# Optimization experiments

Hardware: AMD Instinct MI355X
Metric: run time of the kernel (lower is better)

The kernel has to match this reference:

```python
import jax, jax.numpy as jnp
import numpy as np
from jax import lax

B, ROWS, COLS, K, LATENT = 8, 1536, 16, 32, 16
EPS_REG = 0.01  # torchsort regularization_strength
BIG = 1e30


def setup_inputs() -> dict:
    key = jax.random.key(0)
    ks = jax.random.split(key, 12)
    def w(k, shape):
        return (jax.random.normal(k, shape, jnp.float32) / np.sqrt(shape[0])).astype(jnp.float32)
    return {
        "table": jax.random.uniform(ks[0], (B, ROWS, COLS), jnp.float32),
        "enc_w1": w(ks[1], (COLS, 32)), "enc_b1": 0.01 * jax.random.normal(ks[2], (32,), jnp.float32),
        "enc_w2": w(ks[3], (32, 64)),   "enc_b2": 0.01 * jax.random.normal(ks[4], (64,), jnp.float32),
        "mean_w": w(ks[5], (64, LATENT)), "mean_b": 0.01 * jax.random.normal(ks[6], (LATENT,), jnp.float32),
        "dec_w1": w(ks[7], (LATENT, 32)), "dec_b1": 0.01 * jax.random.normal(ks[8], (32,), jnp.float32),
        "dec_w2": w(ks[9], (32, COLS)),   "dec_b2": 0.01 * jax.random.normal(ks[10], (COLS,), jnp.float32),
        "labels": jax.random.randint(ks[11], (ROWS,), 0, K, jnp.int32),
        "BlockSize": 64,
        "current_epoch": 0,
        "baseline": 0,
    }


def _soft_rank_l2(s, eps):
    # Exact soft_rank (Blondel et al. / torchsort, l2 reg, ascending):
    # project s/eps onto permutahedron of (n,...,1).
    n = s.shape[0]
    x = s / eps
    perm = jnp.argsort(-x)            # descending sort
    xs = x[perm]
    w = jnp.arange(n, 0, -1, dtype=x.dtype)
    # dual = non-increasing isotonic fit of y = xs - w == -iso_inc(-(xs - w))
    y = -(xs - w)
    S = jnp.concatenate([jnp.zeros((1,), x.dtype), jnp.cumsum(y)])
    idx = jnp.arange(n)
    length = jnp.maximum(idx[None, :] - idx[:, None] + 1, 1).astype(x.dtype)
    A = (S[1:][None, :] - S[:n][:, None]) / length           # mean(y[j..k])  [j,k]
    A = jnp.where(idx[None, :] >= idx[:, None], A, BIG)
    Bm = lax.cummin(A, axis=1, reverse=True)                  # min_{k>=i} A[j,k]
    Cm = lax.cummax(Bm, axis=0)                               # max_{j<=i} ...
    iso_inc = jnp.diagonal(Cm)
    dual = -iso_inc
    primal = xs - dual
    inv = jnp.argsort(perm)
    return primal[inv]


def _forward(table, enc_w1, enc_b1, enc_w2, enc_b2, mean_w, mean_b,
             dec_w1, dec_b1, dec_w2, dec_b2, labels, BlockSize):
    b = table.shape[0]
    # VAE (autoencoder path; z = latent mean)
    h = jax.nn.relu(table @ enc_w1 + enc_b1)
    h = jax.nn.relu(h @ enc_w2 + enc_b2)
    z = h @ mean_w + mean_b                                   # [B, rows, 16]
    r = jax.nn.relu(z @ dec_w1 + dec_b1)
    recon = jax.nn.relu(r @ dec_w2 + dec_b2)
    loss = jnp.mean((recon - table) ** 2)
    # clustering scores (labels fixed from batch 0, shared across batch)
    onehot = jax.nn.one_hot(labels, K, dtype=z.dtype)         # [rows, K]
    counts = jnp.maximum(onehot.sum(0), 1.0)                  # [K]
    centers = jnp.einsum('brd,rk->bkd', z, onehot) / counts[None, :, None]
    center_data = centers[:, labels, :]                       # gather back [B, rows, 16]
    d2 = jnp.mean((z - center_data) ** 2, axis=-1)            # [B, rows]
    mn = d2.min(axis=1, keepdims=True); mx = d2.max(axis=1, keepdims=True)
    d2 = (d2 - mn) / (mx - mn)
    scores = d2 + labels.astype(z.dtype)[None, :]
    # training branch
    smn = scores.min(axis=1, keepdims=True); smx = scores.max(axis=1, keepdims=True)
    scaled = (scores - smn) / (smx - smn) * jnp.asarray(b, z.dtype)  # * len(table)
    ranks = jax.vmap(lambda s: _soft_rank_l2(s, EPS_REG))(scaled)
    rank_idx = jnp.argsort(jnp.argsort(scores, axis=1), axis=1) // BlockSize + 1
    rows = table.shape[1]
    return (ranks.reshape(b, rows, 1), rank_idx.reshape(b, rows, 1),
            scores.reshape(b, rows, 1), loss)


def reference(table, enc_w1, enc_b1, enc_w2, enc_b2, mean_w, mean_b,
              dec_w1, dec_b1, dec_w2, dec_b2, labels, BlockSize,
              current_epoch, baseline):
    return _forward(table, enc_w1, enc_b1, enc_w2, enc_b2, mean_w, mean_b,
                    dec_w1, dec_b1, dec_w2, dec_b2, labels, BlockSize)
```

## Files before the change

### kernel.cpp

```cpp
#include <hip/hip_runtime.h>

#define BATCH 8
#define ROWS 1536
#define KCLS 32
#define NTOT (BATCH*ROWS)
#define ELEMS (NTOT*16)
#define SSTRIDE 3073
#define BIGF 1.0e30f

enum : int {
  WS_Z     = 0,
  WS_X     = WS_Z + NTOT*16,
  WS_XS    = WS_X + NTOT,
  WS_S     = WS_XS + NTOT,
  WS_DESC  = WS_S + BATCH*SSTRIDE,
  WS_ASCP  = WS_DESC + NTOT,
  WS_DSCP  = WS_ASCP + 4*NTOT,
  WS_GPART = WS_DSCP + 4*NTOT,
  WS_LOSSP = WS_GPART + BATCH*8*ROWS,
};
#define WS_CPART WS_GPART

#define LW1  0
#define LB1  512
#define LW2  544
#define LB2  2592
#define LMW  2656
#define LMB  3680
#define LDW1 3696
#define LDB1 4208
#define LDW2 4240
#define LDB2 4752
#define LTOT 4768

#define AX   0
#define AH1  16
#define AH2  48
#define AZ   112
#define AR1  128
#define AREC 144
#define ATOT 160
#define ASTRIDE 164

template<int IN_BASE, int IN_N, int OUT_BASE, int OUT_PW, int OUT_TOT,
         int WOFF, int BOFF, bool RELU>
__device__ __forceinline__ void layerw(float* __restrict__ act,
                                       const float* __restrict__ wsh,
                                       int lrow, int wav)
{
  const int o0 = wav * OUT_PW;
  float acc[OUT_PW];
#pragma unroll
  for (int j = 0; j < OUT_PW; ++j) acc[j] = wsh[BOFF + o0 + j];

  const float4* arow = reinterpret_cast<const float4*>(&act[lrow*ASTRIDE + IN_BASE]);
#pragma unroll 2
  for (int i4 = 0; i4 < IN_N/4; ++i4) {
    float4 sv = arow[i4];
    float svx[4];
    svx[0] = sv.x; svx[1] = sv.y; svx[2] = sv.z; svx[3] = sv.w;
#pragma unroll
    for (int u = 0; u < 4; ++u) {
      const float s = svx[u];
      const float4* wp =
        reinterpret_cast<const float4*>(&wsh[WOFF + (i4*4 + u)*OUT_TOT + o0]);
#pragma unroll
      for (int q = 0; q < OUT_PW/4; ++q) {
        float4 w = wp[q];
        acc[q*4+0] = fmaf(s, w.x, acc[q*4+0]);
        acc[q*4+1] = fmaf(s, w.y, acc[q*4+1]);
        acc[q*4+2] = fmaf(s, w.z, acc[q*4+2]);
        acc[q*4+3] = fmaf(s, w.w, acc[q*4+3]);
      }
    }
  }
  float4* orow = reinterpret_cast<float4*>(&act[lrow*ASTRIDE + OUT_BASE + o0]);
#pragma unroll
  for (int q = 0; q < OUT_PW/4; ++q) {
    float4 v;
    v.x = RELU ? fmaxf(acc[q*4+0], 0.f) : acc[q*4+0];
    v.y = RELU ? fmaxf(acc[q*4+1], 0.f) : acc[q*4+1];
    v.z = RELU ? fmaxf(acc[q*4+2], 0.f) : acc[q*4+2];
    v.w = RELU ? fmaxf(acc[q*4+3], 0.f) : acc[q*4+3];
    orow[q] = v;
  }
}

__global__ __launch_bounds__(256, 2) void k1_ae(
    const float* __restrict__ table,
    const float* __restrict__ w1, const float* __restrict__ b1,
    const float* __restrict__ w2, const float* __restrict__ b2,
    const float* __restrict__ mw, const float* __restrict__ mb,
    const float* __restrict__ dw1, const float* __restrict__ db1,
    const float* __restrict__ dw2, const float* __restrict__ db2,
    const int* __restrict__ labels,
    float* __restrict__ ws)
{
  const int tid  = threadIdx.x;
  const int lrow = tid & 63;
  const int wav  = tid >> 6;
  const int blk  = blockIdx.x;
  const int b    = blk / 24;
  const int ch   = blk % 24;

  __shared__ float wsh[LTOT];
  __shared__ float act[64 * ASTRIDE];
  __shared__ int   lbl[64];
  __shared__ float lred[4];

  {
    float4* d4 = reinterpret_cast<float4*>(wsh);
#define CPY(off, src, nf4) \
    { const float4* p = reinterpret_cast<const float4*>(src); \
      for (int t = tid; t < (nf4); t += 256) d4[(off)/4 + t] = p[t]; }
    CPY(LW1,  w1,  128) CPY(LB1,  b1,  8)  CPY(LW2,  w2,  512)
    CPY(LB2,  b2,  16)  CPY(LMW,  mw,  256) CPY(LMB,  mb,  4)
    CPY(LDW1, dw1, 128) CPY(LDB1, db1, 8)  CPY(LDW2, dw2, 128)
    CPY(LDB2, db2, 4)
#undef CPY
    if (tid < 64) lbl[tid] = labels[ch * 64 + tid];
    const float4* tp = reinterpret_cast<const float4*>(table) + blk*256 + tid;
    float4* a4 = reinterpret_cast<float4*>(act);
    a4[(tid >> 2) * (ASTRIDE/4) + (tid & 3)] = *tp;
  }
  __syncthreads();

  layerw<AX,  16, AH1,  8, 32, LW1,  LB1,  true >(act, wsh, lrow, wav);
  __syncthreads();
  layerw<AH1, 32, AH2, 16, 64, LW2,  LB2,  true >(act, wsh, lrow, wav);
  __syncthreads();
  layerw<AH2, 64, AZ,   4, 16, LMW,  LMB,  false>(act, wsh, lrow, wav);
  __syncthreads();

  {
    const float4* a4 = reinterpret_cast<const float4*>(act);
    float4 zv = a4[(tid >> 2) * (ASTRIDE/4) + (AZ/4) + (tid & 3)];
    reinterpret_cast<float4*>(ws + WS_Z)[blk*256 + tid] = zv;
  }

  layerw<AZ,  16, AR1,  8, 32, LDW1, LDB1, true >(act, wsh, lrow, wav);
  __syncthreads();
  layerw<AR1, 32, AREC, 4, 16, LDW2, LDB2, true >(act, wsh, lrow, wav);
  __syncthreads();

  {
    const float4* arow4 = reinterpret_cast<const float4*>(&act[lrow*ASTRIDE]);
    float4 rc = arow4[AREC/4 + wav];
    float4 xv = arow4[AX/4 + wav];
    float d0 = rc.x - xv.x, d1 = rc.y - xv.y, d2 = rc.z - xv.z, d3 = rc.w - xv.w;
    float ls = d0*d0 + d1*d1 + d2*d2 + d3*d3;
    for (int off = 32; off > 0; off >>= 1) ls += __shfl_down(ls, off);
    if (lrow == 0) lred[wav] = ls;
    __syncthreads();
    if (tid == 0) ws[WS_LOSSP + blk] = (lred[0] + lred[1]) + (lred[2] + lred[3]);
  }

  {
    float a0 = 0.f, a1 = 0.f;
    const int d0 = tid & 15,        k0 = tid >> 4;
    const int k1c = k0 + 16;
    for (int rr = 0; rr < 64; ++rr) {
      const int lb = lbl[rr];
      const float zv = act[rr*ASTRIDE + AZ + d0];
      a0 += (lb == k0)  ? zv : 0.f;
      a1 += (lb == k1c) ? zv : 0.f;
    }
    ws[WS_CPART + (b*24 + ch)*512 + tid]       = a0;
    ws[WS_CPART + (b*24 + ch)*512 + 256 + tid] = a1;
  }
}

__global__ __launch_bounds__(256) void k345(const int* __restrict__ labels,
                                            float* __restrict__ ws,
                                            float* __restrict__ out)
{
  const int b = blockIdx.x;
  const int tid = threadIdx.x;
  __shared__ int cnt[KCLS];
  __shared__ float cent[512];
  __shared__ float rmn[256], rmx[256];
  __shared__ int lbl_l[ROWS];

  rmn[tid] = (tid < 192) ? ws[WS_LOSSP + tid] : 0.f;
  if (tid < KCLS) cnt[tid] = 0;
  __syncthreads();
  for (int off = 128; off > 0; off >>= 1) {
    if (tid < off) rmn[tid] += rmn[tid + off];
    __syncthreads();
  }
  if (b == 0 && tid == 0) out[3*NTOT] = rmn[0] / (float)ELEMS;

#pragma unroll
  for (int c = 0; c < 6; ++c) {
    int lb = labels[c*256 + tid];
    lbl_l[c*256 + tid] = lb;
    atomicAdd(&cnt[lb], 1);
  }
  __syncthreads();
#pragma unroll
  for (int e = tid; e < 512; e += 256) {
    float s = 0.f;
#pragma unroll
    for (int c = 0; c < 24; ++c) s += ws[WS_CPART + (b*24 + c)*512 + e];
    const int cn = cnt[e >> 4] > 1 ? cnt[e >> 4] : 1;
    cent[e] = s / (float)cn;
  }
  __syncthreads();

  float d2v[6];
  float tmn = 3.0e38f, tmx = -3.0e38f;
#pragma unroll
  for (int c = 0; c < 6; ++c) {
    const int r = c*256 + tid;
    const int lb = lbl_l[r];
    const float4* zp = reinterpret_cast<const float4*>(ws + WS_Z + (b*ROWS + r)*16);
    const float4* cp = reinterpret_cast<const float4*>(&cent[lb*16]);
    float s = 0.f;
#pragma unroll
    for (int q = 0; q < 4; ++q) {
      float4 zv = zp[q], cv = cp[q];
      float d0 = zv.x - cv.x, d1 = zv.y - cv.y, d2_ = zv.z - cv.z, d3 = zv.w - cv.w;
      s += d0*d0 + d1*d1 + d2_*d2_ + d3*d3;
    }
    d2v[c] = s / 16.f;
    tmn = fminf(tmn, d2v[c]); tmx = fmaxf(tmx, d2v[c]);
  }
  rmn[tid] = tmn; rmx[tid] = tmx;
  __syncthreads();
  for (int off = 128; off > 0; off >>= 1) {
    if (tid < off) {
      rmn[tid] = fminf(rmn[tid], rmn[tid + off]);
      rmx[tid] = fmaxf(rmx[tid], rmx[tid + off]);
    }
    __syncthreads();
  }
  const float mn = rmn[0], mx = rmx[0];
  __syncthreads();

  float sv[6];
  tmn = 3.0e38f; tmx = -3.0e38f;
#pragma unroll
  for (int c = 0; c < 6; ++c) {
    const int r = c*256 + tid;
    float sc = (d2v[c] - mn) / (mx - mn) + (float)lbl_l[r];
    sv[c] = sc;
    out[2*NTOT + b*ROWS + r] = sc;
    tmn = fminf(tmn, sc); tmx = fmaxf(tmx, sc);
  }
  rmn[tid] = tmn; rmx[tid] = tmx;
  __syncthreads();
  for (int off = 128; off > 0; off >>= 1) {
    if (tid < off) {
      rmn[tid] = fminf(rmn[tid], rmn[tid + off]);
      rmx[tid] = fmaxf(rmx[tid], rmx[tid + off]);
    }
    __syncthreads();
  }
  const float smn = rmn[0], smx = rmx[0];
#pragma unroll
  for (int c = 0; c < 6; ++c) {
    const int r = c*256 + tid;
    float scl = (sv[c] - smn) / (smx - smn) * 8.0f;
    ws[WS_X + b*ROWS + r] = scl / 0.01f;
  }
}

__global__ __launch_bounds__(256) void k6_count(float* __restrict__ ws,
                                                const float* __restrict__ out)
{
  const int bi = blockIdx.x;
  const int jb = bi & 3, rb = (bi >> 2) % 6, b = bi / 24;
  const int tid = threadIdx.x;
  __shared__ float4 sld[96], xld[96];
  {
    float* sf = reinterpret_cast<float*>(sld);
    float* xf = reinterpret_cast<float*>(xld);
    const int base = b*ROWS + jb*384;
    sf[tid] = out[2*NTOT + base + tid];
    xf[tid] = ws[WS_X + base + tid];
    if (tid < 128) {
      sf[256 + tid] = out[2*NTOT + base + 256 + tid];
      xf[256 + tid] = ws[WS_X + base + 256 + tid];
    }
  }
  __syncthreads();
  const int r = rb*256 + tid;
  const float si = out[2*NTOT + b*ROWS + r];
  const float xi = ws[WS_X + b*ROWS + r];
  int asc = 0, dsc = 0;
  const int j0 = jb*384;
#pragma unroll 4
  for (int kk = 0; kk < 96; ++kk) {
    const float4 s4 = sld[kk];
    const float4 x4 = xld[kk];
    const int j = j0 + kk*4;
    asc += (s4.x < si || (s4.x == si && j   < r)) ? 1 : 0;
    asc += (s4.y < si || (s4.y == si && j+1 < r)) ? 1 : 0;
    asc += (s4.z < si || (s4.z == si && j+2 < r)) ? 1 : 0;
    asc += (s4.w < si || (s4.w == si && j+3 < r)) ? 1 : 0;
    dsc += (x4.x > xi || (x4.x == xi && j   < r)) ? 1 : 0;
    dsc += (x4.y > xi || (x4.y == xi && j+1 < r)) ? 1 : 0;
    dsc += (x4.z > xi || (x4.z == xi && j+2 < r)) ? 1 : 0;
    dsc += (x4.w > xi || (x4.w == xi && j+3 < r)) ? 1 : 0;
  }
  int* wsi = reinterpret_cast<int*>(ws);
  wsi[WS_ASCP + jb*NTOT + b*ROWS + r] = asc;
  wsi[WS_DSCP + jb*NTOT + b*ROWS + r] = dsc;
}

__global__ __launch_bounds__(256) void k67(const int* __restrict__ bsp,
                                           float* __restrict__ ws,
                                           float* __restrict__ out)
{
  const int b = blockIdx.x, tid = threadIdx.x;
  __shared__ float xs_l[ROWS];
  __shared__ float ts[256];
  const int* wsi = reinterpret_cast<const int*>(ws);
  int* wsw = reinterpret_cast<int*>(ws);
  const int BS = *bsp;
#pragma unroll
  for (int c = 0; c < 6; ++c) {
    const int r = c*256 + tid;
    const int idx = b*ROWS + r;
    int asc = 0, dsc = 0;
#pragma unroll
    for (int jb = 0; jb < 4; ++jb) {
      asc += wsi[WS_ASCP + jb*NTOT + idx];
      dsc += wsi[WS_DSCP + jb*NTOT + idx];
    }
    out[NTOT + idx] = (float)(asc / BS + 1);
    wsw[WS_DESC + idx] = dsc;
    xs_l[dsc] = ws[WS_X + idx];
  }
  __syncthreads();
  const int base = tid * 6;
  float y[6], sum = 0.f;
#pragma unroll
  for (int u = 0; u < 6; ++u) {
    ws[WS_XS + b*ROWS + base + u] = xs_l[base + u];
    y[u] = (float)(ROWS - (base + u)) - xs_l[base + u];
    sum += y[u];
  }
  ts[tid] = sum;
  __syncthreads();
  for (int off = 1; off < 256; off <<= 1) {
    float v = ts[tid];
    if (tid >= off) v += ts[tid - off];
    __syncthreads();
    ts[tid] = v;
    __syncthreads();
  }
  float run = tid ? ts[tid - 1] : 0.f;
  float* S = ws + WS_S + b*SSTRIDE;
#pragma unroll
  for (int u = 0; u < 6; ++u) { S[base + u] = run; run += y[u]; }
  if (tid == 255) S[ROWS] = run;
#pragma unroll
  for (int u = 0; u < 6; ++u) S[ROWS + 1 + tid*6 + u] = BIGF;
}

__global__ __launch_bounds__(256) void k8a(float* __restrict__ ws)
{
  const int bi = blockIdx.x;
  const int c = bi & 7, ib = (bi >> 3) % 6, b = bi / 48;
  const int tid = threadIdx.x;
  __shared__ float Sseg[448];
  __shared__ float invl[192];
  const float* S = ws + WS_S + b*SSTRIDE;
  const int ibase = ib*256;
  const int segbase = ibase + c*192 + 1;
  Sseg[tid] = S[segbase + tid];
  if (tid < 192) {
    Sseg[256 + tid] = S[segbase + 256 + tid];
    invl[tid] = 1.0f / (float)(c*192 + tid + 1);
  }
  __syncthreads();
  const int i = ibase + tid;
  const float Si = S[i];
  float gm = 3.0e38f;
#pragma unroll 8
  for (int k = 0; k < 192; ++k)
    gm = fminf(gm, (Sseg[tid + k] - Si) * invl[k]);
  ws[WS_GPART + (b*8 + c)*ROWS + i] = gm;
}

__global__ __launch_bounds__(768) void k8b(float* __restrict__ ws,
                                           float* __restrict__ out)
{
  const int b = blockIdx.x, tid = threadIdx.x;
  __shared__ float g[ROWS];
  __shared__ float pm[768];
  for (int t = tid; t < ROWS; t += 768) {
    float gm = 3.0e38f;
#pragma unroll
    for (int c = 0; c < 8; ++c)
      gm = fminf(gm, ws[WS_GPART + (b*8 + c)*ROWS + t]);
    g[t] = gm;
  }
  __syncthreads();
  const float a = g[2*tid], cc = g[2*tid + 1];
  pm[tid] = fmaxf(a, cc);
  __syncthreads();
  for (int off = 1; off < 768; off <<= 1) {
    float v = pm[tid];
    if (tid >= off) v = fmaxf(v, pm[tid - off]);
    __syncthreads();
    pm[tid] = v;
    __syncthreads();
  }
  const float excl = tid ? pm[tid - 1] : -3.0e38f;
  const float i0 = fmaxf(excl, a);
  const float i1 = fmaxf(i0, cc);
  g[2*tid] = i0; g[2*tid + 1] = i1;
  __syncthreads();
  const float* xs = ws + WS_XS + b*ROWS;
  const int* desc = reinterpret_cast<const int*>(ws) + WS_DESC + b*ROWS;
  for (int t = tid; t < ROWS; t += 768) {
    const int dr = desc[t];
    out[b*ROWS + t] = xs[dr] + g[dr];
  }
}

extern "C" void kernel_launch(void* const* d_in, const int* in_sizes, int n_in,
                              void* d_out, int out_size, void* d_ws, size_t ws_size,
                              hipStream_t stream) {
  const float* table = (const float*)d_in[0];
  const float* w1  = (const float*)d_in[1];
  const float* b1  = (const float*)d_in[2];
  const float* w2  = (const float*)d_in[3];
  const float* b2  = (const float*)d_in[4];
  const float* mw  = (const float*)d_in[5];
  const float* mb  = (const float*)d_in[6];
  const float* dw1 = (const float*)d_in[7];
  const float* db1 = (const float*)d_in[8];
  const float* dw2 = (const float*)d_in[9];
  const float* db2 = (const float*)d_in[10];
  const int* labels = (const int*)d_in[11];
  const int* bsp    = (const int*)d_in[12];
  float* out = (float*)d_out;
  float* ws  = (float*)d_ws;

  k1_ae<<<192, 256, 0, stream>>>(table, w1, b1, w2, b2, mw, mb, dw1, db1, dw2, db2, labels, ws);
  k345<<<8, 256, 0, stream>>>(labels, ws, out);
  k6_count<<<192, 256, 0, stream>>>(ws, out);
  k67<<<8, 256, 0, stream>>>(bsp, ws, out);
  k8a<<<384, 256, 0, stream>>>(ws);
  k8b<<<8, 768, 0, stream>>>(ws, out);
}
```

Before: 62.71 us.

## Split autoencoder kernel into 16-row blocks to quadruple grid size

The autoencoder kernel now handles 16 rows per block with 16 threads per output slice, instead of 64 rows with 4 waves, so it launches 768 blocks rather than 192. The aim is to fill more of the GPU's compute units and shorten the per-block serial work in the small MLP layers. In exchange, every block reloads the full weight set into shared memory, and the downstream kernel has to sum 96 per-chunk centroid partials and 768 loss partials instead of 24 and 192. The workspace layout grows to hold the extra partial sums.

```diff
diff --git a/kernel.cpp b/kernel.cpp
--- a/kernel.cpp
+++ b/kernel.cpp
@@ -17,7 +17,7 @@
   WS_ASCP  = WS_DESC + NTOT,
   WS_DSCP  = WS_ASCP + 4*NTOT,
   WS_GPART = WS_DSCP + 4*NTOT,
-  WS_LOSSP = WS_GPART + BATCH*8*ROWS,
+  WS_LOSSP = WS_GPART + BATCH*96*512,
 };
 #define WS_CPART WS_GPART
 
@@ -42,13 +42,16 @@
 #define ATOT 160
 #define ASTRIDE 164
 
+#define RPB 16
+#define FWAYS 16
+
 template<int IN_BASE, int IN_N, int OUT_BASE, int OUT_PW, int OUT_TOT,
          int WOFF, int BOFF, bool RELU>
 __device__ __forceinline__ void layerw(float* __restrict__ act,
                                        const float* __restrict__ wsh,
-                                       int lrow, int wav)
-{
-  const int o0 = wav * OUT_PW;
+                                       int lrow, int fway)
+{
+  const int o0 = fway * OUT_PW;
   float acc[OUT_PW];
 #pragma unroll
   for (int j = 0; j < OUT_PW; ++j) acc[j] = wsh[BOFF + o0 + j];
@@ -62,31 +65,47 @@
 #pragma unroll
     for (int u = 0; u < 4; ++u) {
       const float s = svx[u];
-      const float4* wp =
-        reinterpret_cast<const float4*>(&wsh[WOFF + (i4*4 + u)*OUT_TOT + o0]);
-#pragma unroll
-      for (int q = 0; q < OUT_PW/4; ++q) {
-        float4 w = wp[q];
-        acc[q*4+0] = fmaf(s, w.x, acc[q*4+0]);
-        acc[q*4+1] = fmaf(s, w.y, acc[q*4+1]);
-        acc[q*4+2] = fmaf(s, w.z, acc[q*4+2]);
-        acc[q*4+3] = fmaf(s, w.w, acc[q*4+3]);
+      const float* wp = &wsh[WOFF + (i4*4 + u)*OUT_TOT + o0];
+      if constexpr (OUT_PW == 1) {
+        acc[0] = fmaf(s, wp[0], acc[0]);
+      } else if constexpr (OUT_PW == 2) {
+        float2 w = *reinterpret_cast<const float2*>(wp);
+        acc[0] = fmaf(s, w.x, acc[0]);
+        acc[1] = fmaf(s, w.y, acc[1]);
+      } else {
+#pragma unroll
+        for (int q = 0; q < OUT_PW/4; ++q) {
+          float4 w = reinterpret_cast<const float4*>(wp)[q];
+          acc[q*4+0] = fmaf(s, w.x, acc[q*4+0]);
+          acc[q*4+1] = fmaf(s, w.y, acc[q*4+1]);
+          acc[q*4+2] = fmaf(s, w.z, acc[q*4+2]);
+          acc[q*4+3] = fmaf(s, w.w, acc[q*4+3]);
+        }
       }
     }
   }
-  float4* orow = reinterpret_cast<float4*>(&act[lrow*ASTRIDE + OUT_BASE + o0]);
-#pragma unroll
-  for (int q = 0; q < OUT_PW/4; ++q) {
-    float4 v;
-    v.x = RELU ? fmaxf(acc[q*4+0], 0.f) : acc[q*4+0];
-    v.y = RELU ? fmaxf(acc[q*4+1], 0.f) : acc[q*4+1];
-    v.z = RELU ? fmaxf(acc[q*4+2], 0.f) : acc[q*4+2];
-    v.w = RELU ? fmaxf(acc[q*4+3], 0.f) : acc[q*4+3];
-    orow[q] = v;
-  }
-}
-
-__global__ __launch_bounds__(256, 2) void k1_ae(
+  float* orow = &act[lrow*ASTRIDE + OUT_BASE + o0];
+  if constexpr (OUT_PW == 1) {
+    orow[0] = RELU ? fmaxf(acc[0], 0.f) : acc[0];
+  } else if constexpr (OUT_PW == 2) {
+    float2 v;
+    v.x = RELU ? fmaxf(acc[0], 0.f) : acc[0];
+    v.y = RELU ? fmaxf(acc[1], 0.f) : acc[1];
+    *reinterpret_cast<float2*>(orow) = v;
+  } else {
+#pragma unroll
+    for (int q = 0; q < OUT_PW/4; ++q) {
+      float4 v;
+      v.x = RELU ? fmaxf(acc[q*4+0], 0.f) : acc[q*4+0];
+      v.y = RELU ? fmaxf(acc[q*4+1], 0.f) : acc[q*4+1];
+      v.z = RELU ? fmaxf(acc[q*4+2], 0.f) : acc[q*4+2];
+      v.w = RELU ? fmaxf(acc[q*4+3], 0.f) : acc[q*4+3];
+      reinterpret_cast<float4*>(orow)[q] = v;
+    }
+  }
+}
+
+__global__ __launch_bounds__(256, 4) void k1_ae(
     const float* __restrict__ table,
     const float* __restrict__ w1, const float* __restrict__ b1,
     const float* __restrict__ w2, const float* __restrict__ b2,
@@ -97,15 +116,15 @@
     float* __restrict__ ws)
 {
   const int tid  = threadIdx.x;
-  const int lrow = tid & 63;
-  const int wav  = tid >> 6;
+  const int lrow = tid & (RPB-1);
+  const int fway = tid >> 4;
   const int blk  = blockIdx.x;
-  const int b    = blk / 24;
-  const int ch   = blk % 24;
+  const int b    = blk / 96;
+  const int ch   = blk % 96;
 
   __shared__ float wsh[LTOT];
-  __shared__ float act[64 * ASTRIDE];
-  __shared__ int   lbl[64];
+  __shared__ float act[RPB * ASTRIDE];
+  __shared__ int   lbl[RPB];
   __shared__ float lred[4];
 
   {
@@ -118,55 +137,54 @@
     CPY(LDW1, dw1, 128) CPY(LDB1, db1, 8)  CPY(LDW2, dw2, 128)
     CPY(LDB2, db2, 4)
 #undef CPY
-    if (tid < 64) lbl[tid] = labels[ch * 64 + tid];
-    const float4* tp = reinterpret_cast<const float4*>(table) + blk*256 + tid;
-    float4* a4 = reinterpret_cast<float4*>(act);
-    a4[(tid >> 2) * (ASTRIDE/4) + (tid & 3)] = *tp;
-  }
-  __syncthreads();
-
-  layerw<AX,  16, AH1,  8, 32, LW1,  LB1,  true >(act, wsh, lrow, wav);
-  __syncthreads();
-  layerw<AH1, 32, AH2, 16, 64, LW2,  LB2,  true >(act, wsh, lrow, wav);
-  __syncthreads();
-  layerw<AH2, 64, AZ,   4, 16, LMW,  LMB,  false>(act, wsh, lrow, wav);
+    if (tid < RPB) lbl[tid] = labels[ch * RPB + tid];
+    if (tid < RPB*4) {
+      const float4 v = reinterpret_cast<const float4*>(table)[blk*(RPB*4) + tid];
+      reinterpret_cast<float4*>(act)[(tid >> 2)*(ASTRIDE/4) + (tid & 3)] = v;
+    }
+  }
+  __syncthreads();
+
+  layerw<AX,  16, AH1, 2, 32, LW1,  LB1,  true >(act, wsh, lrow, fway);
+  __syncthreads();
+  layerw<AH1, 32, AH2, 4, 64, LW2,  LB2,  true >(act, wsh, lrow, fway);
+  __syncthreads();
+  layerw<AH2, 64, AZ,  1, 16, LMW,  LMB,  false>(act, wsh, lrow, fway);
+  __syncthreads();
+
+  if (tid < RPB*4) {
+    const float4 zv =
+      reinterpret_cast<const float4*>(act)[(tid >> 2)*(ASTRIDE/4) + (AZ/4) + (tid & 3)];
+    reinterpret_cast<float4*>(ws + WS_Z)[blk*(RPB*4) + tid] = zv;
+  }
+
+  layerw<AZ,  16, AR1, 2, 32, LDW1, LDB1, true >(act, wsh, lrow, fway);
+  __syncthreads();
+  layerw<AR1, 32, AREC,1, 16, LDW2, LDB2, true >(act, wsh, lrow, fway);
   __syncthreads();
 
   {
-    const float4* a4 = reinterpret_cast<const float4*>(act);
-    float4 zv = a4[(tid >> 2) * (ASTRIDE/4) + (AZ/4) + (tid & 3)];
-    reinterpret_cast<float4*>(ws + WS_Z)[blk*256 + tid] = zv;
-  }
-
-  layerw<AZ,  16, AR1,  8, 32, LDW1, LDB1, true >(act, wsh, lrow, wav);
-  __syncthreads();
-  layerw<AR1, 32, AREC, 4, 16, LDW2, LDB2, true >(act, wsh, lrow, wav);
-  __syncthreads();
-
-  {
-    const float4* arow4 = reinterpret_cast<const float4*>(&act[lrow*ASTRIDE]);
-    float4 rc = arow4[AREC/4 + wav];
-    float4 xv = arow4[AX/4 + wav];
-    float d0 = rc.x - xv.x, d1 = rc.y - xv.y, d2 = rc.z - xv.z, d3 = rc.w - xv.w;
-    float ls = d0*d0 + d1*d1 + d2*d2 + d3*d3;
+    const float d = act[lrow*ASTRIDE + AREC + fway] - act[lrow*ASTRIDE + AX + fway];
+    float ls = d * d;
     for (int off = 32; off > 0; off >>= 1) ls += __shfl_down(ls, off);
-    if (lrow == 0) lred[wav] = ls;
+    if ((tid & 63) == 0) lred[tid >> 6] = ls;
     __syncthreads();
     if (tid == 0) ws[WS_LOSSP + blk] = (lred[0] + lred[1]) + (lred[2] + lred[3]);
   }
 
   {
     float a0 = 0.f, a1 = 0.f;
-    const int d0 = tid & 15,        k0 = tid >> 4;
+    const int d0 = tid & 15, k0 = tid >> 4;
     const int k1c = k0 + 16;
-    for (int rr = 0; rr < 64; ++rr) {
+#pragma unroll
+    for (int rr = 0; rr < RPB; ++rr) {
       const int lb = lbl[rr];
       const float zv = act[rr*ASTRIDE + AZ + d0];
       a0 += (lb == k0)  ? zv : 0.f;
       a1 += (lb == k1c) ? zv : 0.f;
     }
-    ws[WS_CPART + (b*24 + ch)*512 + tid]       = a0;
-    ws[WS_CPART + (b*24 + ch)*512 + 256 + tid] = a1;
+    ws[WS_CPART + (b*96 + ch)*512 + tid]       = a0;
+    ws[WS_CPART + (b*96 + ch)*512 + 256 + tid] = a1;
   }
 }
 
@@ -181,7 +199,7 @@
   __shared__ float rmn[256], rmx[256];
   __shared__ int lbl_l[ROWS];
 
-  rmn[tid] = (tid < 192) ? ws[WS_LOSSP + tid] : 0.f;
+  rmn[tid] = ws[WS_LOSSP + tid] + ws[WS_LOSSP + 256 + tid] + ws[WS_LOSSP + 512 + tid];
   if (tid < KCLS) cnt[tid] = 0;
   __syncthreads();
   for (int off = 128; off > 0; off >>= 1) {
@@ -200,8 +218,7 @@
 #pragma unroll
   for (int e = tid; e < 512; e += 256) {
     float s = 0.f;
-#pragma unroll
-    for (int c = 0; c < 24; ++c) s += ws[WS_CPART + (b*24 + c)*512 + e];
+    for (int c = 0; c < 96; ++c) s += ws[WS_CPART + (b*96 + c)*512 + e];
     const int cn = cnt[e >> 4] > 1 ? cnt[e >> 4] : 1;
     cent[e] = s / (float)cn;
   }
@@ -440,7 +457,7 @@
   float* out = (float*)d_out;
   float* ws  = (float*)d_ws;
 
-  k1_ae<<<192, 256, 0, stream>>>(table, w1, b1, w2, b2, mw, mb, dw1, db1, dw2, db2, labels, ws);
+  k1_ae<<<768, 256, 0, stream>>>(table, w1, b1, w2, b2, mw, mb, dw1, db1, dw2, db2, labels, ws);
   k345<<<8, 256, 0, stream>>>(labels, ws, out);
   k6_count<<<192, 256, 0, stream>>>(ws, out);
   k67<<<8, 256, 0, stream>>>(bsp, ws, out);
```

Result: slower. 66.26 us (+5.7%).
